# Optimization experiments

Measured on AMD Instinct MI355X. Metric: run time of the kernel, lower is better.

The kernel has to match this reference:

```python
import jax, jax.numpy as jnp
import numpy as np

N = 100000      # nodes
E = 1600000     # edges
F_IN, H1, H2, H3, F_OUT = 64, 128, 128, 64, 8


def _lin(key, fan_in, fan_out):
    return jax.random.normal(key, (fan_in, fan_out), jnp.float32) / np.sqrt(fan_in).astype(np.float32)


def setup_inputs() -> dict:
    key = jax.random.key(0)
    ks = jax.random.split(key, 16)
    x = jax.random.normal(ks[0], (N, F_IN), jnp.float32)
    edge_index = jax.random.randint(ks[1], (2, E), 0, N, dtype=jnp.int64)
    return {
        "x": x,
        "edge_index": edge_index,
        "eps1": jnp.zeros((), jnp.float32),
        "eps2": jnp.zeros((), jnp.float32),
        "eps3": jnp.zeros((), jnp.float32),
        "W1a": _lin(ks[2], F_IN, H1), "b1a": jnp.zeros((H1,), jnp.float32),
        "W1b": _lin(ks[3], H1, H1),   "b1b": jnp.zeros((H1,), jnp.float32),
        "W2a": _lin(ks[4], H1, H2),   "b2a": jnp.zeros((H2,), jnp.float32),
        "W2b": _lin(ks[5], H2, H2),   "b2b": jnp.zeros((H2,), jnp.float32),
        "W3a": _lin(ks[6], H2, H3),   "b3a": jnp.zeros((H3,), jnp.float32),
        "W3b": _lin(ks[7], H3, H3),   "b3b": jnp.zeros((H3,), jnp.float32),
        "Wfc": _lin(ks[8], H3, F_OUT), "bfc": jnp.zeros((F_OUT,), jnp.float32),
    }


def _gin_conv(x, src, dst, eps, Wa, ba, Wb, bb):
    # out_i = MLP((1+eps) * x_i + sum_{j in N(i)} x_j)
    agg = jax.ops.segment_sum(x[src], dst, num_segments=N)  # scatter-add over edges
    h = (1.0 + eps) * x + agg
    return jax.nn.relu(h @ Wa + ba) @ Wb + bb


def reference(x, edge_index, eps1, eps2, eps3,
              W1a, b1a, W1b, b1b,
              W2a, b2a, W2b, b2b,
              W3a, b3a, W3b, b3b,
              Wfc, bfc):
    src, dst = edge_index[0], edge_index[1]
    x = jax.nn.relu(_gin_conv(x, src, dst, eps1, W1a, b1a, W1b, b1b))
    x = jax.nn.relu(_gin_conv(x, src, dst, eps2, W2a, b2a, W2b, b2b))
    x = jax.nn.relu(_gin_conv(x, src, dst, eps3, W3a, b3a, W3b, b3b))
    emb = jax.lax.stop_gradient(x)  # x.clone().detach()
    out = x @ Wfc + bfc
    return out, emb
```

## Files before the change

### kernel.cpp

```cpp
#include <hip/hip_runtime.h>
#include <hip/hip_bf16.h>
#include <stdint.h>

typedef unsigned short ushort_t;
typedef __attribute__((ext_vector_type(8))) short short8;
typedef __attribute__((ext_vector_type(4))) float floatx4;

__device__ __forceinline__ float bf2f(unsigned short u){
  union { unsigned int i; float f; } v; v.i = ((unsigned int)u) << 16; return v.f;
}
__device__ __forceinline__ unsigned short f2bf(float f){
  union { float f; unsigned int i; } v; v.f = f;
  unsigned int r = v.i + 0x7FFFu + ((v.i >> 16) & 1u);
  return (unsigned short)(r >> 16);
}
__device__ __forceinline__ unsigned int pack2(unsigned short lo, unsigned short hi){
  return ((unsigned int)hi << 16) | (unsigned int)lo;
}


__global__ __launch_bounds__(256) void k_detect(const unsigned int* __restrict__ w, int* __restrict__ flag){
  int t = threadIdx.x;
  unsigned int acc = 0;
  #pragma unroll
  for (int i=0;i<16;++i) acc |= w[2*(t*16+i)+1];
  #pragma unroll
  for (int o=32;o>=1;o>>=1) acc |= __shfl_xor(acc, o);
  if ((t&63)==0 && acc) atomicOr(flag, 1);
}


__global__ __launch_bounds__(256) void k_bhist(const unsigned int* __restrict__ w, const int* __restrict__ mode,
                                               int* __restrict__ ghist, int E, int N){
  __shared__ int h[256];
  int t = threadIdx.x;
  h[t] = 0; __syncthreads();
  int m = *mode;
  int base = blockIdx.x*4096 + t;
  #pragma unroll
  for (int i=0;i<16;++i){
    int e = base + i*256;
    if (e < E){
      int d = m ? (int)w[(size_t)E + e] : (int)w[2*((size_t)E + e)];
      if ((unsigned)d < (unsigned)N) atomicAdd(&h[d>>9], 1);
    }
  }
  __syncthreads();
  if (h[t]) atomicAdd(&ghist[t], h[t]);
}

__global__ __launch_bounds__(256) void k_bscan(const int* __restrict__ ghist, int* __restrict__ bbase,
                                               int* __restrict__ gcur, int NB){
  __shared__ int sv[256];
  int t = threadIdx.x;
  int v = (t < NB) ? ghist[t] : 0;
  sv[t] = v; __syncthreads();
  for (int o=1;o<256;o<<=1){
    int xv = (t>=o)? sv[t-o] : 0;
    __syncthreads();
    sv[t] += xv;
    __syncthreads();
  }
  int excl = sv[t] - v;
  if (t < NB){ bbase[t] = excl; gcur[t] = excl; }
  if (t == NB-1) bbase[NB] = excl + v;
}

__global__ __launch_bounds__(256) void k_bin(const unsigned int* __restrict__ w, const int* __restrict__ mode,
                                             int* __restrict__ gcur, int2* __restrict__ pairs,
                                             int E, int N, int NB){
  __shared__ int h[256];
  __shared__ int cur[256];
  int t = threadIdx.x;
  h[t] = 0; __syncthreads();
  int m = *mode;
  int base = blockIdx.x*4096 + t;
  int d[16], s[16];
  #pragma unroll
  for (int i=0;i<16;++i){
    int e = base + i*256;
    d[i] = -1; s[i] = 0;
    if (e < E){
      if (m){ s[i] = (int)w[e];           d[i] = (int)w[(size_t)E + e]; }
      else  { s[i] = (int)w[2*(size_t)e]; d[i] = (int)w[2*((size_t)E + e)]; }
      if ((unsigned)d[i] >= (unsigned)N || (unsigned)s[i] >= (unsigned)N) d[i] = -1;
    }
  }
  #pragma unroll
  for (int i=0;i<16;++i)
    if (d[i] >= 0) atomicAdd(&h[d[i]>>9], 1);
  __syncthreads();
  if (t < NB && h[t]) cur[t] = atomicAdd(&gcur[t], h[t]);
  __syncthreads();
  #pragma unroll
  for (int i=0;i<16;++i){
    if (d[i] >= 0){
      int p = atomicAdd(&cur[d[i]>>9], 1);
      pairs[p] = make_int2(d[i], s[i]);
    }
  }
}

__global__ __launch_bounds__(256) void k_bcsr(const int2* __restrict__ pairs, const int* __restrict__ bbase,
                                              int* __restrict__ offs, int* __restrict__ csr, int N, int NB){
  __shared__ int cnt[512];
  __shared__ int wsum[4];
  int b = blockIdx.x, t = threadIdx.x, lane = t&63, wv = t>>6;
  int lo = bbase[b], hi = bbase[b+1];
  int node0 = b << 9;
  cnt[t] = 0; cnt[t+256] = 0;
  __syncthreads();
  for (int i = lo+t; i < hi; i += 256){
    int2 p = pairs[i];
    atomicAdd(&cnt[p.x - node0], 1);
  }
  __syncthreads();
  int v0 = cnt[2*t], v1 = cnt[2*t+1], tot = v0+v1;
  int s = tot;
  #pragma unroll
  for (int o=1;o<64;o<<=1){ int xv = __shfl_up(s,o); if (lane>=o) s += xv; }
  if (lane==63) wsum[wv] = s;
  __syncthreads();
  int basev = 0;
  for (int j=0;j<wv;++j) basev += wsum[j];
  int excl = basev + s - tot;
  int e0 = lo + excl, e1 = lo + excl + v0;
  cnt[2*t] = e0; cnt[2*t+1] = e1;
  int n0 = node0 + 2*t, n1 = node0 + 2*t + 1;
  if (n0 < N) offs[n0] = e0;
  if (n1 < N) offs[n1] = e1;
  if (b == NB-1 && t == 255) offs[N] = hi;
  __syncthreads();
  for (int i = lo+t; i < hi; i += 256){
    int2 p = pairs[i];
    int pos = atomicAdd(&cnt[p.x - node0], 1);
    csr[pos] = p.y;
  }
}


__global__ __launch_bounds__(256) void k_perm(const float* W1a, const float* W1b, const float* W2a,
                                              const float* W2b, const float* W3a, const float* W3b,
                                              const float* Wfc, ushort_t* out){
  int id = blockIdx.x*256 + threadIdx.x;
  const float* src; int K, M, base, local;
  if      (id <  8192){ src=W1a; K=64;  M=128; base=0;     local=id; }
  else if (id < 24576){ src=W1b; K=128; M=128; base=8192;  local=id-8192; }
  else if (id < 40960){ src=W2a; K=128; M=128; base=24576; local=id-24576; }
  else if (id < 57344){ src=W2b; K=128; M=128; base=40960; local=id-40960; }
  else if (id < 65536){ src=W3a; K=128; M=64;  base=57344; local=id-57344; }
  else if (id < 69632){ src=W3b; K=64;  M=64;  base=65536; local=id-65536; }
  else if (id < 70656){ src=Wfc; K=64;  M=16;  base=69632; local=id-69632; }
  else return;
  int k = local / M, nn = local - k*M;
  float val;
  if (src == Wfc) val = (nn<8) ? Wfc[k*8+nn] : 0.0f;
  else            val = src[k*M+nn];
  int idx = (((nn>>4)*(K/32) + (k>>5))*4 + ((k>>3)&3))*128 + (nn&15)*8 + (k&7);
  out[base+idx] = f2bf(val);
}


__global__ __launch_bounds__(256) void k_tobf(const float2* __restrict__ xin, unsigned int* __restrict__ xb, int total2){
  int i = blockIdx.x*256 + threadIdx.x;
  if (i < total2){
    float2 v = xin[i];
    xb[i] = pack2(f2bf(v.x), f2bf(v.y));
  }
}


template<int F>
__global__ __launch_bounds__(256) void k_gatherx(const uint2* __restrict__ xr, const int* __restrict__ offs,
                                                 const int* __restrict__ csr, const float* __restrict__ epsp,
                                                 uint2* __restrict__ hr, int n){
  constexpr int G = F/4;
  constexpr int NPW = 64/(2*G);
  int gt = blockIdx.x*256 + threadIdx.x;
  int wv = gt >> 6, lane = gt & 63;
  int grp  = lane / (2*G);
  int half = (lane / G) & 1;
  int f    = lane % G;
  int node = wv*NPW + grp;
  if (node >= n) return;
  const size_t row = (size_t)node*G;
  uint2 sv = xr[row + f];
  float e1s = 1.0f + epsp[0];
  float a0, a1, a2, a3;
  if (half == 0){
    a0 = e1s*bf2f((ushort_t)(sv.x & 0xffffu)); a1 = e1s*bf2f((ushort_t)(sv.x >> 16));
    a2 = e1s*bf2f((ushort_t)(sv.y & 0xffffu)); a3 = e1s*bf2f((ushort_t)(sv.y >> 16));
  } else { a0 = a1 = a2 = a3 = 0.f; }
  int u0 = offs[node], u1 = offs[node+1];
  int u = u0;
#define ACC4(v) { a0 += bf2f((ushort_t)((v).x & 0xffffu)); a1 += bf2f((ushort_t)((v).x >> 16)); \
                  a2 += bf2f((ushort_t)((v).y & 0xffffu)); a3 += bf2f((ushort_t)((v).y >> 16)); }
  for (; u+7 < u1; u += 8){
    int s0 = csr[u   + half];
    int s1 = csr[u+2 + half];
    int s2 = csr[u+4 + half];
    int s3 = csr[u+6 + half];
    uint2 v0 = xr[(size_t)s0*G + f];
    uint2 v1 = xr[(size_t)s1*G + f];
    uint2 v2 = xr[(size_t)s2*G + f];
    uint2 v3 = xr[(size_t)s3*G + f];
    ACC4(v0) ACC4(v1) ACC4(v2) ACC4(v3)
  }
  for (; u+1 < u1; u += 2){
    int s = csr[u + half];
    uint2 v = xr[(size_t)s*G + f];
    ACC4(v)
  }
  if (u < u1 && half == 0){
    int s = csr[u];
    uint2 v = xr[(size_t)s*G + f];
    ACC4(v)
  }
#undef ACC4
  a0 += __shfl_xor(a0, G);
  a1 += __shfl_xor(a1, G);
  a2 += __shfl_xor(a2, G);
  a3 += __shfl_xor(a3, G);
  if (half == 0){
    uint2 o2;
    o2.x = pack2(f2bf(a0), f2bf(a1));
    o2.y = pack2(f2bf(a2), f2bf(a3));
    hr[row + f] = o2;
  }
}


template<int F, int M1, int M2, bool LAST>
__global__ __launch_bounds__(256)
void k_mlp(const ushort_t* __restrict__ h,
           const ushort_t* __restrict__ wp1, const float* __restrict__ b1,
           const ushort_t* __restrict__ wp2, const float* __restrict__ b2,
           ushort_t* __restrict__ xout,
           float* __restrict__ embp,
           const ushort_t* __restrict__ wpfc, const float* __restrict__ bfc,
           float* __restrict__ outp, int n)
{
  constexpr int NT1 = M1/16, NT2 = M2/16, KC1 = F/32, KC2 = M1/32;
  __shared__ short sC1[4*(M1/8)*136];
  __shared__ short sX3[LAST ? (4*8*136) : 1];
  int tid = threadIdx.x, lane = tid&63, w = tid>>6;
  int m16 = lane&15, quad = lane>>4;
  int row0 = blockIdx.x*64 + w*16;
  size_t arow = (size_t)(row0 + m16);

  floatx4 acc[NT1];
  #pragma unroll
  for (int i=0;i<NT1;++i) acc[i] = (floatx4){0.f,0.f,0.f,0.f};
  #pragma unroll
  for (int kc=0; kc<KC1; ++kc){
    short8 a = *(const short8*)(h + arow*F + kc*32 + quad*8);
    #pragma unroll
    for (int nt=0; nt<NT1; ++nt){
      short8 b = *(const short8*)(wp1 + (size_t)((nt*KC1+kc)*64 + lane)*8);
      acc[nt] = __builtin_amdgcn_mfma_f32_16x16x32_bf16(a, b, acc[nt], 0, 0, 0);
    }
  }
  #pragma unroll
  for (int nt=0; nt<NT1; ++nt){
    int c = nt*16 + m16;
    float bias = b1[c];
    #pragma unroll
    for (int r=0;r<4;++r){
      float v = fmaxf(acc[nt][r] + bias, 0.f);
      int mm = quad*4 + r;
      sC1[(w*(M1/8) + (c>>3))*136 + mm*8 + (c&7)] = (short)f2bf(v);
    }
  }
  __syncthreads();

  floatx4 acc2[NT2];
  #pragma unroll
  for (int i=0;i<NT2;++i) acc2[i] = (floatx4){0.f,0.f,0.f,0.f};
  #pragma unroll
  for (int kc=0; kc<KC2; ++kc){
    short8 a = *(const short8*)&sC1[(w*(M1/8) + kc*4 + quad)*136 + m16*8];
    #pragma unroll
    for (int nt=0; nt<NT2; ++nt){
      short8 b = *(const short8*)(wp2 + (size_t)((nt*KC2+kc)*64 + lane)*8);
      acc2[nt] = __builtin_amdgcn_mfma_f32_16x16x32_bf16(a, b, acc2[nt], 0, 0, 0);
    }
  }
  #pragma unroll
  for (int nt=0; nt<NT2; ++nt){
    int c = nt*16 + m16;
    float bias = b2[c];
    #pragma unroll
    for (int r=0;r<4;++r){
      float v = fmaxf(acc2[nt][r] + bias, 0.f);
      int mm = quad*4 + r;
      int row = row0 + mm;
      if constexpr (!LAST){
        if (row < n) xout[(size_t)row*M2 + c] = f2bf(v);
      } else {
        if (row < n) embp[(size_t)row*64 + c] = v;
        sX3[(w*8 + (c>>3))*136 + mm*8 + (c&7)] = (short)f2bf(v);
      }
    }
  }

  if constexpr (LAST){
    __syncthreads();
    floatx4 accf = (floatx4){0.f,0.f,0.f,0.f};
    #pragma unroll
    for (int kc=0; kc<2; ++kc){
      short8 a = *(const short8*)&sX3[(w*8 + kc*4 + quad)*136 + m16*8];
      short8 b = *(const short8*)(wpfc + (size_t)(kc*64 + lane)*8);
      accf = __builtin_amdgcn_mfma_f32_16x16x32_bf16(a, b, accf, 0, 0, 0);
    }
    if (m16 < 8){
      float bias = bfc[m16];
      #pragma unroll
      for (int r=0;r<4;++r){
        int row = row0 + quad*4 + r;
        if (row < n) outp[(size_t)row*8 + m16] = accf[r] + bias;
      }
    }
  }
}


extern "C" void kernel_launch(void* const* d_in, const int* in_sizes, int n_in,
                              void* d_out, int out_size, void* d_ws, size_t ws_size,
                              hipStream_t stream)
{
  const int N = in_sizes[0] / 64;
  const int E = in_sizes[1] / 2;
  const int NB = (N + 511) / 512;
  const float*        x    = (const float*)d_in[0];
  const unsigned int* ew   = (const unsigned int*)d_in[1];
  const float* eps1 = (const float*)d_in[2];
  const float* eps2 = (const float*)d_in[3];
  const float* eps3 = (const float*)d_in[4];
  const float* W1a  = (const float*)d_in[5];
  const float* b1a  = (const float*)d_in[6];
  const float* W1b  = (const float*)d_in[7];
  const float* b1b  = (const float*)d_in[8];
  const float* W2a  = (const float*)d_in[9];
  const float* b2a  = (const float*)d_in[10];
  const float* W2b  = (const float*)d_in[11];
  const float* b2b  = (const float*)d_in[12];
  const float* W3a  = (const float*)d_in[13];
  const float* b3a  = (const float*)d_in[14];
  const float* W3b  = (const float*)d_in[15];
  const float* b3b  = (const float*)d_in[16];
  const float* Wfc  = (const float*)d_in[17];
  const float* bfc  = (const float*)d_in[18];

  float* outp = (float*)d_out;
  float* emb  = outp + (size_t)N*8;

  const int Npad = ((N + 63)/64)*64;

  char* ws = (char*)d_ws;
  size_t o = 0;
  auto alloc = [&](size_t bytes)->char* {
    char* p = ws + o;
    o = (o + bytes + 255) & ~(size_t)255;
    return p;
  };
  int*      mode  = (int*)alloc(4);
  int*      ghist = (int*)alloc(256*4);
  int*      bbase = (int*)alloc(257*4);
  int*      gcur  = (int*)alloc(256*4);
  int*      offs  = (int*)alloc((size_t)(N+1)*4);
  int2*     pairs = (int2*)alloc((size_t)E*8);
  int*      csr   = (int*)alloc((size_t)E*4);
  ushort_t* wperm = (ushort_t*)alloc(70656ull*2);
  ushort_t* xb    = (ushort_t*)alloc((size_t)Npad*64*2);
  ushort_t* hbuf  = (ushort_t*)alloc((size_t)Npad*128*2);
  ushort_t* x1    = (ushort_t*)alloc((size_t)Npad*128*2);

  hipMemsetAsync(mode, 0, 4, stream);
  hipMemsetAsync(ghist, 0, 256*4, stream);
  k_detect<<<1, 256, 0, stream>>>(ew, mode);
  const int nbB = (E + 4095)/4096;
  k_bhist<<<nbB, 256, 0, stream>>>(ew, mode, ghist, E, N);
  k_bscan<<<1, 256, 0, stream>>>(ghist, bbase, gcur, NB);
  k_bin<<<nbB, 256, 0, stream>>>(ew, mode, gcur, pairs, E, N, NB);
  k_bcsr<<<NB, 256, 0, stream>>>(pairs, bbase, offs, csr, N, NB);
  k_perm<<<(70656+255)/256, 256, 0, stream>>>(W1a, W1b, W2a, W2b, W3a, W3b, Wfc, wperm);
  k_tobf<<<(N*32+255)/256, 256, 0, stream>>>((const float2*)x, (unsigned int*)xb, N*32);

  k_gatherx<64><<<(((N+1)/2)+3)/4, 256, 0, stream>>>((const uint2*)xb, offs, csr, eps1,
                                                     (uint2*)hbuf, N);
  k_mlp<64,128,128,false><<<Npad/64, 256, 0, stream>>>(hbuf, wperm+0, b1a, wperm+8192, b1b,
                                                       x1, nullptr, nullptr, nullptr, nullptr, N);
  k_gatherx<128><<<(N+3)/4, 256, 0, stream>>>((const uint2*)x1, offs, csr, eps2,
                                              (uint2*)hbuf, N);
  k_mlp<128,128,128,false><<<Npad/64, 256, 0, stream>>>(hbuf, wperm+24576, b2a, wperm+40960, b2b,
                                                        x1, nullptr, nullptr, nullptr, nullptr, N);
  k_gatherx<128><<<(N+3)/4, 256, 0, stream>>>((const uint2*)x1, offs, csr, eps3,
                                              (uint2*)hbuf, N);
  k_mlp<128,64,64,true><<<Npad/64, 256, 0, stream>>>(hbuf, wperm+57344, b3a, wperm+65536, b3b,
                                                     nullptr, emb, wperm+69632, bfc, outp, N);
}
```

Measured before the change: 424.7 us.

## Fuse neighbor aggregation into GIN MLP kernel via shared-memory staging

```diff
diff --git a/kernel.cpp b/kernel.cpp
--- a/kernel.cpp
+++ b/kernel.cpp
@@ -170,90 +170,89 @@
 }
 
 
-template<int F>
-__global__ __launch_bounds__(256) void k_gatherx(const uint2* __restrict__ xr, const int* __restrict__ offs,
-                                                 const int* __restrict__ csr, const float* __restrict__ epsp,
-                                                 uint2* __restrict__ hr, int n){
-  constexpr int G = F/4;
-  constexpr int NPW = 64/(2*G);
-  int gt = blockIdx.x*256 + threadIdx.x;
-  int wv = gt >> 6, lane = gt & 63;
-  int grp  = lane / (2*G);
-  int half = (lane / G) & 1;
-  int f    = lane % G;
-  int node = wv*NPW + grp;
-  if (node >= n) return;
-  const size_t row = (size_t)node*G;
-  uint2 sv = xr[row + f];
-  float e1s = 1.0f + epsp[0];
-  float a0, a1, a2, a3;
-  if (half == 0){
-    a0 = e1s*bf2f((ushort_t)(sv.x & 0xffffu)); a1 = e1s*bf2f((ushort_t)(sv.x >> 16));
-    a2 = e1s*bf2f((ushort_t)(sv.y & 0xffffu)); a3 = e1s*bf2f((ushort_t)(sv.y >> 16));
-  } else { a0 = a1 = a2 = a3 = 0.f; }
-  int u0 = offs[node], u1 = offs[node+1];
-  int u = u0;
-#define ACC4(v) { a0 += bf2f((ushort_t)((v).x & 0xffffu)); a1 += bf2f((ushort_t)((v).x >> 16)); \
-                  a2 += bf2f((ushort_t)((v).y & 0xffffu)); a3 += bf2f((ushort_t)((v).y >> 16)); }
-  for (; u+7 < u1; u += 8){
-    int s0 = csr[u   + half];
-    int s1 = csr[u+2 + half];
-    int s2 = csr[u+4 + half];
-    int s3 = csr[u+6 + half];
-    uint2 v0 = xr[(size_t)s0*G + f];
-    uint2 v1 = xr[(size_t)s1*G + f];
-    uint2 v2 = xr[(size_t)s2*G + f];
-    uint2 v3 = xr[(size_t)s3*G + f];
-    ACC4(v0) ACC4(v1) ACC4(v2) ACC4(v3)
-  }
-  for (; u+1 < u1; u += 2){
-    int s = csr[u + half];
-    uint2 v = xr[(size_t)s*G + f];
-    ACC4(v)
-  }
-  if (u < u1 && half == 0){
-    int s = csr[u];
-    uint2 v = xr[(size_t)s*G + f];
-    ACC4(v)
-  }
-#undef ACC4
-  a0 += __shfl_xor(a0, G);
-  a1 += __shfl_xor(a1, G);
-  a2 += __shfl_xor(a2, G);
-  a3 += __shfl_xor(a3, G);
-  if (half == 0){
-    uint2 o2;
-    o2.x = pack2(f2bf(a0), f2bf(a1));
-    o2.y = pack2(f2bf(a2), f2bf(a3));
-    hr[row + f] = o2;
-  }
-}
-
-
 template<int F, int M1, int M2, bool LAST>
 __global__ __launch_bounds__(256)
-void k_mlp(const ushort_t* __restrict__ h,
-           const ushort_t* __restrict__ wp1, const float* __restrict__ b1,
-           const ushort_t* __restrict__ wp2, const float* __restrict__ b2,
-           ushort_t* __restrict__ xout,
-           float* __restrict__ embp,
-           const ushort_t* __restrict__ wpfc, const float* __restrict__ bfc,
-           float* __restrict__ outp, int n)
+void k_gmlp(const uint2* __restrict__ xr, const int* __restrict__ offs,
+            const int* __restrict__ csr, const float* __restrict__ epsp,
+            const ushort_t* __restrict__ wp1, const float* __restrict__ b1,
+            const ushort_t* __restrict__ wp2, const float* __restrict__ b2,
+            ushort_t* __restrict__ xout,
+            float* __restrict__ embp,
+            const ushort_t* __restrict__ wpfc, const float* __restrict__ bfc,
+            float* __restrict__ outp, int n)
 {
   constexpr int NT1 = M1/16, NT2 = M2/16, KC1 = F/32, KC2 = M1/32;
+  constexpr int G2 = F/4;
+  constexpr int NG = 64/G2;
+  __shared__ ushort_t hA[64][F+8];
   __shared__ short sC1[4*(M1/8)*136];
   __shared__ short sX3[LAST ? (4*8*136) : 1];
   int tid = threadIdx.x, lane = tid&63, w = tid>>6;
   int m16 = lane&15, quad = lane>>4;
   int row0 = blockIdx.x*64 + w*16;
-  size_t arow = (size_t)(row0 + m16);
+
+  {
+    int grp = lane / G2, f = lane % G2;
+    float e1s = 1.0f + epsp[0];
+#define ACC4(v) { a0 += bf2f((ushort_t)((v).x & 0xffffu)); a1 += bf2f((ushort_t)((v).x >> 16)); \
+                  a2 += bf2f((ushort_t)((v).y & 0xffffu)); a3 += bf2f((ushort_t)((v).y >> 16)); }
+    for (int i=0;i<16;++i){
+      int node = row0 + i;
+      float a0=0.f, a1=0.f, a2=0.f, a3=0.f;
+      if (node < n){
+        if (grp == 0){
+          uint2 sv = xr[(size_t)node*G2 + f];
+          a0 = e1s*bf2f((ushort_t)(sv.x & 0xffffu)); a1 = e1s*bf2f((ushort_t)(sv.x >> 16));
+          a2 = e1s*bf2f((ushort_t)(sv.y & 0xffffu)); a3 = e1s*bf2f((ushort_t)(sv.y >> 16));
+        }
+        int u0 = offs[node], u1 = offs[node+1];
+        int u = u0;
+        for (; u + 4*NG-1 < u1; u += 4*NG){
+          int s0 = csr[u        + grp];
+          int s1 = csr[u +   NG + grp];
+          int s2 = csr[u + 2*NG + grp];
+          int s3 = csr[u + 3*NG + grp];
+          uint2 v0 = xr[(size_t)s0*G2 + f];
+          uint2 v1 = xr[(size_t)s1*G2 + f];
+          uint2 v2 = xr[(size_t)s2*G2 + f];
+          uint2 v3 = xr[(size_t)s3*G2 + f];
+          ACC4(v0) ACC4(v1) ACC4(v2) ACC4(v3)
+        }
+        for (; u + NG-1 < u1; u += NG){
+          int s = csr[u + grp];
+          uint2 v = xr[(size_t)s*G2 + f];
+          ACC4(v)
+        }
+        if (u + grp < u1){
+          int s = csr[u + grp];
+          uint2 v = xr[(size_t)s*G2 + f];
+          ACC4(v)
+        }
+      }
+      #pragma unroll
+      for (int off=G2; off<64; off<<=1){
+        a0 += __shfl_xor(a0, off);
+        a1 += __shfl_xor(a1, off);
+        a2 += __shfl_xor(a2, off);
+        a3 += __shfl_xor(a3, off);
+      }
+      if (grp == 0){
+        uint2 o2;
+        o2.x = pack2(f2bf(a0), f2bf(a1));
+        o2.y = pack2(f2bf(a2), f2bf(a3));
+        *(uint2*)&hA[w*16 + i][f*4] = o2;
+      }
+    }
+#undef ACC4
+  }
+  __syncthreads();
 
   floatx4 acc[NT1];
   #pragma unroll
   for (int i=0;i<NT1;++i) acc[i] = (floatx4){0.f,0.f,0.f,0.f};
   #pragma unroll
   for (int kc=0; kc<KC1; ++kc){
-    short8 a = *(const short8*)(h + arow*F + kc*32 + quad*8);
+    short8 a = *(const short8*)&hA[w*16 + m16][kc*32 + quad*8];
     #pragma unroll
     for (int nt=0; nt<NT1; ++nt){
       short8 b = *(const short8*)(wp1 + (size_t)((nt*KC1+kc)*64 + lane)*8);
@@ -372,8 +371,8 @@
   int*      csr   = (int*)alloc((size_t)E*4);
   ushort_t* wperm = (ushort_t*)alloc(70656ull*2);
   ushort_t* xb    = (ushort_t*)alloc((size_t)Npad*64*2);
-  ushort_t* hbuf  = (ushort_t*)alloc((size_t)Npad*128*2);
   ushort_t* x1    = (ushort_t*)alloc((size_t)Npad*128*2);
+  ushort_t* x2    = (ushort_t*)alloc((size_t)Npad*128*2);
 
   hipMemsetAsync(mode, 0, 4, stream);
   hipMemsetAsync(ghist, 0, 256*4, stream);
@@ -386,16 +385,14 @@
   k_perm<<<(70656+255)/256, 256, 0, stream>>>(W1a, W1b, W2a, W2b, W3a, W3b, Wfc, wperm);
   k_tobf<<<(N*32+255)/256, 256, 0, stream>>>((const float2*)x, (unsigned int*)xb, N*32);
 
-  k_gatherx<64><<<(((N+1)/2)+3)/4, 256, 0, stream>>>((const uint2*)xb, offs, csr, eps1,
-                                                     (uint2*)hbuf, N);
-  k_mlp<64,128,128,false><<<Npad/64, 256, 0, stream>>>(hbuf, wperm+0, b1a, wperm+8192, b1b,
-                                                       x1, nullptr, nullptr, nullptr, nullptr, N);
-  k_gatherx<128><<<(N+3)/4, 256, 0, stream>>>((const uint2*)x1, offs, csr, eps2,
-                                              (uint2*)hbuf, N);
-  k_mlp<128,128,128,false><<<Npad/64, 256, 0, stream>>>(hbuf, wperm+24576, b2a, wperm+40960, b2b,
-                                                        x1, nullptr, nullptr, nullptr, nullptr, N);
-  k_gatherx<128><<<(N+3)/4, 256, 0, stream>>>((const uint2*)x1, offs, csr, eps3,
-                                              (uint2*)hbuf, N);
-  k_mlp<128,64,64,true><<<Npad/64, 256, 0, stream>>>(hbuf, wperm+57344, b3a, wperm+65536, b3b,
-                                                     nullptr, emb, wperm+69632, bfc, outp, N);
-}
+  const int gblk = (N + 63)/64;
+  k_gmlp<64,128,128,false><<<gblk, 256, 0, stream>>>((const uint2*)xb, offs, csr, eps1,
+                                                     wperm+0, b1a, wperm+8192, b1b,
+                                                     x1, nullptr, nullptr, nullptr, nullptr, N);
+  k_gmlp<128,128,128,false><<<gblk, 256, 0, stream>>>((const uint2*)x1, offs, csr, eps2,
+                                                      wperm+24576, b2a, wperm+40960, b2b,
+                                                      x2, nullptr, nullptr, nullptr, nullptr, N);
+  k_gmlp<128,64,64,true><<<gblk, 256, 0, stream>>>((const uint2*)x2, offs, csr, eps3,
+                                                   wperm+57344, b3a, wperm+65536, b3b,
+                                                   nullptr, emb, wperm+69632, bfc, outp, N);
+}
```

After: 545.2 us. 1.28x slower.

## Fuse preprocessing kernels into one launch and unroll gather loop deeper

Applied to the files above, without the earlier changes.

```diff
diff --git a/kernel.cpp b/kernel.cpp
--- a/kernel.cpp
+++ b/kernel.cpp
@@ -17,37 +17,74 @@
 __device__ __forceinline__ unsigned int pack2(unsigned short lo, unsigned short hi){
   return ((unsigned int)hi << 16) | (unsigned int)lo;
 }
-
-
-__global__ __launch_bounds__(256) void k_detect(const unsigned int* __restrict__ w, int* __restrict__ flag){
-  int t = threadIdx.x;
-  unsigned int acc = 0;
-  #pragma unroll
-  for (int i=0;i<16;++i) acc |= w[2*(t*16+i)+1];
-  #pragma unroll
-  for (int o=32;o>=1;o>>=1) acc |= __shfl_xor(acc, o);
-  if ((t&63)==0 && acc) atomicOr(flag, 1);
-}
-
-
-__global__ __launch_bounds__(256) void k_bhist(const unsigned int* __restrict__ w, const int* __restrict__ mode,
-                                               int* __restrict__ ghist, int E, int N){
-  __shared__ int h[256];
-  int t = threadIdx.x;
-  h[t] = 0; __syncthreads();
-  int m = *mode;
-  int base = blockIdx.x*4096 + t;
-  #pragma unroll
-  for (int i=0;i<16;++i){
-    int e = base + i*256;
-    if (e < E){
-      int d = m ? (int)w[(size_t)E + e] : (int)w[2*((size_t)E + e)];
-      if ((unsigned)d < (unsigned)N) atomicAdd(&h[d>>9], 1);
-    }
-  }
-  __syncthreads();
-  if (h[t]) atomicAdd(&ghist[t], h[t]);
-}
+__device__ __forceinline__ float bflo(unsigned int v){
+  union { unsigned int u; float f; } c; c.u = v << 16; return c.f;
+}
+__device__ __forceinline__ float bfhi(unsigned int v){
+  union { unsigned int u; float f; } c; c.u = v & 0xffff0000u; return c.f;
+}
+
+
+__global__ __launch_bounds__(256)
+void k_prep(const unsigned int* __restrict__ w, int* __restrict__ ghist, int E, int N, int nbB,
+            const float2* __restrict__ xin, unsigned int* __restrict__ xb, int total2, int tobfB,
+            const float* __restrict__ W1a, const float* __restrict__ W1b, const float* __restrict__ W2a,
+            const float* __restrict__ W2b, const float* __restrict__ W3a, const float* __restrict__ W3b,
+            const float* __restrict__ Wfc, ushort_t* __restrict__ wout)
+{
+  int b = blockIdx.x, t = threadIdx.x;
+  if (b < nbB){
+    __shared__ int h[256];
+    __shared__ unsigned int dred[4];
+    h[t] = 0;
+    int base = b*4096 + t;
+    unsigned int acc = 0;
+    #pragma unroll
+    for (int i=0;i<16;++i){
+      int e = base + i*256;
+      if (e < E) acc |= w[2*e+1];
+    }
+    #pragma unroll
+    for (int o=32;o>=1;o>>=1) acc |= __shfl_xor(acc, o);
+    if ((t&63)==0) dred[t>>6] = acc;
+    __syncthreads();
+    int m = (dred[0]|dred[1]|dred[2]|dred[3]) != 0;
+    #pragma unroll
+    for (int i=0;i<16;++i){
+      int e = base + i*256;
+      if (e < E){
+        int d = m ? (int)w[(size_t)E + e] : (int)w[2*((size_t)E + e)];
+        if ((unsigned)d < (unsigned)N) atomicAdd(&h[d>>9], 1);
+      }
+    }
+    __syncthreads();
+    if (h[t]) atomicAdd(&ghist[t], h[t]);
+  } else if (b < nbB + tobfB){
+    int i = (b - nbB)*256 + t;
+    if (i < total2){
+      float2 v = xin[i];
+      xb[i] = pack2(f2bf(v.x), f2bf(v.y));
+    }
+  } else {
+    int id = (b - nbB - tobfB)*256 + t;
+    const float* src; int K, M, base2, local;
+    if      (id <  8192){ src=W1a; K=64;  M=128; base2=0;     local=id; }
+    else if (id < 24576){ src=W1b; K=128; M=128; base2=8192;  local=id-8192; }
+    else if (id < 40960){ src=W2a; K=128; M=128; base2=24576; local=id-24576; }
+    else if (id < 57344){ src=W2b; K=128; M=128; base2=40960; local=id-40960; }
+    else if (id < 65536){ src=W3a; K=128; M=64;  base2=57344; local=id-57344; }
+    else if (id < 69632){ src=W3b; K=64;  M=64;  base2=65536; local=id-65536; }
+    else if (id < 70656){ src=Wfc; K=64;  M=16;  base2=69632; local=id-69632; }
+    else return;
+    int k = local / M, nn = local - k*M;
+    float val;
+    if (src == Wfc) val = (nn<8) ? Wfc[k*8+nn] : 0.0f;
+    else            val = src[k*M+nn];
+    int idx = (((nn>>4)*(K/32) + (k>>5))*4 + ((k>>3)&3))*128 + (nn&15)*8 + (k&7);
+    wout[base2+idx] = f2bf(val);
+  }
+}
+
 
 __global__ __launch_bounds__(256) void k_bscan(const int* __restrict__ ghist, int* __restrict__ bbase,
                                                int* __restrict__ gcur, int NB){
@@ -66,15 +103,26 @@
   if (t == NB-1) bbase[NB] = excl + v;
 }
 
-__global__ __launch_bounds__(256) void k_bin(const unsigned int* __restrict__ w, const int* __restrict__ mode,
+__global__ __launch_bounds__(256) void k_bin(const unsigned int* __restrict__ w,
                                              int* __restrict__ gcur, int2* __restrict__ pairs,
                                              int E, int N, int NB){
   __shared__ int h[256];
   __shared__ int cur[256];
+  __shared__ unsigned int dred[4];
   int t = threadIdx.x;
-  h[t] = 0; __syncthreads();
-  int m = *mode;
+  h[t] = 0;
   int base = blockIdx.x*4096 + t;
+  unsigned int acc = 0;
+  #pragma unroll
+  for (int i=0;i<16;++i){
+    int e = base + i*256;
+    if (e < E) acc |= w[2*e+1];
+  }
+  #pragma unroll
+  for (int o=32;o>=1;o>>=1) acc |= __shfl_xor(acc, o);
+  if ((t&63)==0) dred[t>>6] = acc;
+  __syncthreads();
+  int m = (dred[0]|dred[1]|dred[2]|dred[3]) != 0;
   int d[16], s[16];
   #pragma unroll
   for (int i=0;i<16;++i){
@@ -135,37 +183,6 @@
     int2 p = pairs[i];
     int pos = atomicAdd(&cnt[p.x - node0], 1);
     csr[pos] = p.y;
-  }
-}
-
-
-__global__ __launch_bounds__(256) void k_perm(const float* W1a, const float* W1b, const float* W2a,
-                                              const float* W2b, const float* W3a, const float* W3b,
-                                              const float* Wfc, ushort_t* out){
-  int id = blockIdx.x*256 + threadIdx.x;
-  const float* src; int K, M, base, local;
-  if      (id <  8192){ src=W1a; K=64;  M=128; base=0;     local=id; }
-  else if (id < 24576){ src=W1b; K=128; M=128; base=8192;  local=id-8192; }
-  else if (id < 40960){ src=W2a; K=128; M=128; base=24576; local=id-24576; }
-  else if (id < 57344){ src=W2b; K=128; M=128; base=40960; local=id-40960; }
-  else if (id < 65536){ src=W3a; K=128; M=64;  base=57344; local=id-57344; }
-  else if (id < 69632){ src=W3b; K=64;  M=64;  base=65536; local=id-65536; }
-  else if (id < 70656){ src=Wfc; K=64;  M=16;  base=69632; local=id-69632; }
-  else return;
-  int k = local / M, nn = local - k*M;
-  float val;
-  if (src == Wfc) val = (nn<8) ? Wfc[k*8+nn] : 0.0f;
-  else            val = src[k*M+nn];
-  int idx = (((nn>>4)*(K/32) + (k>>5))*4 + ((k>>3)&3))*128 + (nn&15)*8 + (k&7);
-  out[base+idx] = f2bf(val);
-}
-
-
-__global__ __launch_bounds__(256) void k_tobf(const float2* __restrict__ xin, unsigned int* __restrict__ xb, int total2){
-  int i = blockIdx.x*256 + threadIdx.x;
-  if (i < total2){
-    float2 v = xin[i];
-    xb[i] = pack2(f2bf(v.x), f2bf(v.y));
   }
 }
 
@@ -188,18 +205,27 @@
   float e1s = 1.0f + epsp[0];
   float a0, a1, a2, a3;
   if (half == 0){
-    a0 = e1s*bf2f((ushort_t)(sv.x & 0xffffu)); a1 = e1s*bf2f((ushort_t)(sv.x >> 16));
-    a2 = e1s*bf2f((ushort_t)(sv.y & 0xffffu)); a3 = e1s*bf2f((ushort_t)(sv.y >> 16));
+    a0 = e1s*bflo(sv.x); a1 = e1s*bfhi(sv.x);
+    a2 = e1s*bflo(sv.y); a3 = e1s*bfhi(sv.y);
   } else { a0 = a1 = a2 = a3 = 0.f; }
   int u0 = offs[node], u1 = offs[node+1];
   int u = u0;
-#define ACC4(v) { a0 += bf2f((ushort_t)((v).x & 0xffffu)); a1 += bf2f((ushort_t)((v).x >> 16)); \
-                  a2 += bf2f((ushort_t)((v).y & 0xffffu)); a3 += bf2f((ushort_t)((v).y >> 16)); }
+#define ACC4(v) { a0 += bflo((v).x); a1 += bfhi((v).x); a2 += bflo((v).y); a3 += bfhi((v).y); }
+  for (; u+15 < u1; u += 16){
+    int s0 = csr[u    + half], s1 = csr[u+2  + half], s2 = csr[u+4  + half], s3 = csr[u+6  + half];
+    int s4 = csr[u+8  + half], s5 = csr[u+10 + half], s6 = csr[u+12 + half], s7 = csr[u+14 + half];
+    uint2 v0 = xr[(size_t)s0*G + f];
+    uint2 v1 = xr[(size_t)s1*G + f];
+    uint2 v2 = xr[(size_t)s2*G + f];
+    uint2 v3 = xr[(size_t)s3*G + f];
+    uint2 v4 = xr[(size_t)s4*G + f];
+    uint2 v5 = xr[(size_t)s5*G + f];
+    uint2 v6 = xr[(size_t)s6*G + f];
+    uint2 v7 = xr[(size_t)s7*G + f];
+    ACC4(v0) ACC4(v1) ACC4(v2) ACC4(v3) ACC4(v4) ACC4(v5) ACC4(v6) ACC4(v7)
+  }
   for (; u+7 < u1; u += 8){
-    int s0 = csr[u   + half];
-    int s1 = csr[u+2 + half];
-    int s2 = csr[u+4 + half];
-    int s3 = csr[u+6 + half];
+    int s0 = csr[u + half], s1 = csr[u+2 + half], s2 = csr[u+4 + half], s3 = csr[u+6 + half];
     uint2 v0 = xr[(size_t)s0*G + f];
     uint2 v1 = xr[(size_t)s1*G + f];
     uint2 v2 = xr[(size_t)s2*G + f];
@@ -363,7 +389,6 @@
     o = (o + bytes + 255) & ~(size_t)255;
     return p;
   };
-  int*      mode  = (int*)alloc(4);
   int*      ghist = (int*)alloc(256*4);
   int*      bbase = (int*)alloc(257*4);
   int*      gcur  = (int*)alloc(256*4);
@@ -375,16 +400,16 @@
   ushort_t* hbuf  = (ushort_t*)alloc((size_t)Npad*128*2);
   ushort_t* x1    = (ushort_t*)alloc((size_t)Npad*128*2);
 
-  hipMemsetAsync(mode, 0, 4, stream);
   hipMemsetAsync(ghist, 0, 256*4, stream);
-  k_detect<<<1, 256, 0, stream>>>(ew, mode);
-  const int nbB = (E + 4095)/4096;
-  k_bhist<<<nbB, 256, 0, stream>>>(ew, mode, ghist, E, N);
+  const int nbB   = (E + 4095)/4096;
+  const int tobfB = (N*32 + 255)/256;
+  const int permB = 70656/256;
+  k_prep<<<nbB + tobfB + permB, 256, 0, stream>>>(ew, ghist, E, N, nbB,
+                                                  (const float2*)x, (unsigned int*)xb, N*32, tobfB,
+                                                  W1a, W1b, W2a, W2b, W3a, W3b, Wfc, wperm);
   k_bscan<<<1, 256, 0, stream>>>(ghist, bbase, gcur, NB);
-  k_bin<<<nbB, 256, 0, stream>>>(ew, mode, gcur, pairs, E, N, NB);
+  k_bin<<<nbB, 256, 0, stream>>>(ew, gcur, pairs, E, N, NB);
   k_bcsr<<<NB, 256, 0, stream>>>(pairs, bbase, offs, csr, N, NB);
-  k_perm<<<(70656+255)/256, 256, 0, stream>>>(W1a, W1b, W2a, W2b, W3a, W3b, Wfc, wperm);
-  k_tobf<<<(N*32+255)/256, 256, 0, stream>>>((const float2*)x, (unsigned int*)xb, N*32);
 
   k_gatherx<64><<<(((N+1)/2)+3)/4, 256, 0, stream>>>((const uint2*)xb, offs, csr, eps1,
                                                      (uint2*)hbuf, N);
```

Result: faster. 416.2 us (-2.0%).
